# Kernel optimization log

Measured on AMD Instinct MI355X. Metric: run time of the kernel, lower is better.

Reference implementation:

```python
import jax, jax.numpy as jnp
import numpy as np

EPS_PRE = 1e-05   # constant added to raw scores in the torch module
EPS_NORM = 1e-12  # F.normalize default eps


def setup_inputs() -> dict:
    key = jax.random.key(0)
    kq, kk, kv = jax.random.split(key, 3)
    B, H, S, D = 2, 8, 2048, 64
    query = jax.random.normal(kq, (B, H, S, D), dtype=jnp.float32)
    keys = jax.random.normal(kk, (B, H, S, D), dtype=jnp.float32)
    vals = jax.random.normal(kv, (B, H, S, D), dtype=jnp.float32)
    # causal mask, broadcastable over batch and heads; mask==0 -> score zeroed
    mask = jnp.tril(jnp.ones((S, S), dtype=jnp.int32))[None, None, :, :]
    return {"query": query, "keys": keys, "vals": vals, "mask": mask}


def reference(query, keys, vals, mask):
    # preattn: [B,H,S,S]
    preattn = jnp.einsum("bhsd,bhtd->bhst", query, keys) + EPS_PRE
    preattn = jnp.where(mask == 0, 0.0, preattn)
    # F.normalize(dim=-1): x / max(||x||_2, eps)
    norm = jnp.sqrt(jnp.sum(preattn * preattn, axis=-1, keepdims=True))
    attn = preattn / jnp.maximum(norm, EPS_NORM)
    # dropout is identity in eval mode (reference baseline)
    out = jnp.einsum("bhst,bhtd->bhsd", attn, vals)
    return (out, attn)
```

## Files before the change

kernel.cpp:

```cpp
#include <hip/hip_runtime.h>

#define S_DIM 2048
#define D_DIM 64
#define EPS_PRE 1e-5f
#define EPS_NORM 1e-12f

typedef __attribute__((ext_vector_type(8))) short bf8;
typedef __attribute__((ext_vector_type(4))) float f32x4;

static __device__ __forceinline__ unsigned fbits(float x){ union{float f;unsigned u;}v; v.f=x; return v.u; }
static __device__ __forceinline__ float bcast(unsigned u){ union{unsigned u;float f;}v; v.u=u; return v.f; }

static __device__ __forceinline__ void split2(float x, unsigned short& h, unsigned short& l){
  unsigned u = fbits(x);
  h = (unsigned short)(u >> 16);
  float lo = x - bcast(u & 0xffff0000u);
  l = (unsigned short)(fbits(lo) >> 16);
}

static __device__ __forceinline__ void pack4f(float x0, float x1, float x2, float x3,
                                              uint2& hh, uint2& ll){
  unsigned u0=fbits(x0),u1=fbits(x1),u2=fbits(x2),u3=fbits(x3);
  hh.x = (u0>>16) | (u1 & 0xffff0000u);
  hh.y = (u2>>16) | (u3 & 0xffff0000u);
  float l0 = x0 - bcast(u0&0xffff0000u);
  float l1 = x1 - bcast(u1&0xffff0000u);
  float l2 = x2 - bcast(u2&0xffff0000u);
  float l3 = x3 - bcast(u3&0xffff0000u);
  ll.x = (fbits(l0)>>16) | (fbits(l1)&0xffff0000u);
  ll.y = (fbits(l2)>>16) | (fbits(l3)&0xffff0000u);
}

static __device__ __forceinline__ f32x4 mfma16(bf8 a, bf8 b, f32x4 c){
  return __builtin_amdgcn_mfma_f32_16x16x32_bf16(a, b, c, 0, 0, 0);
}

__global__ __launch_bounds__(256, 2)
void lka_fused(const float* __restrict__ Qg, const float* __restrict__ Kg,
               const float* __restrict__ Vg, float* __restrict__ Og,
               float* __restrict__ Ag)
{
  __shared__ short kThi[4096], kTlo[4096];
  __shared__ short vThi[4096], vTlo[4096];
  __shared__ short pHi [4096], pLo [4096];

  const int tid = threadIdx.x;
  const int wv  = tid >> 6;
  const int ln  = tid & 63;
  const int gq  = ln >> 4;
  const int i16 = ln & 15;

  const int blk = blockIdx.x;
  const int bh  = (blk & 7) | (((blk >> 3) & 1) << 3);
  const int qq  = blk >> 4;
  const int rbk = (qq < 16) ? qq : 47 - qq;
  const int s0  = rbk * 64;

  const float* Qb = Qg + (size_t)bh * (S_DIM * D_DIM);
  const float* Kb = Kg + (size_t)bh * (S_DIM * D_DIM);
  const float* Vb = Vg + (size_t)bh * (S_DIM * D_DIM);
  float* Ob = Og + (size_t)bh * (S_DIM * D_DIM);
  float* Ab = Ag + (size_t)bh * ((size_t)S_DIM * S_DIM);

  const int srow = s0 + wv * 16 + i16;

  bf8 qhi[2], qlo[2];
  #pragma unroll
  for (int ks = 0; ks < 2; ++ks) {
    const float* qp = Qb + (size_t)srow * D_DIM + ks * 32 + gq * 8;
    float4 a = *(const float4*)qp;
    float4 b = *(const float4*)(qp + 4);
    union { bf8 v; unsigned short h[8]; } H, L;
    float f0[8] = {a.x,a.y,a.z,a.w,b.x,b.y,b.z,b.w};
    #pragma unroll
    for (int j = 0; j < 8; ++j) split2(f0[j], H.h[j], L.h[j]);
    qhi[ks] = H.v; qlo[ks] = L.v;
  }

  {
    const int c0 = (rbk + 1) * 64;
    const int n4 = (S_DIM - c0) >> 2;
    const int r  = tid >> 2;
    float* rowp = Ab + (size_t)(s0 + r) * S_DIM + c0;
    float4 z = make_float4(0.f, 0.f, 0.f, 0.f);
    for (int c = (tid & 3); c < n4; c += 4)
      *(float4*)(rowp + 4*c) = z;
  }

  auto stageK = [&](int t0){
    const int t  = tid >> 2;
    const int db = (tid & 3) * 16;
    const float* kp = Kb + (size_t)(t0 + t) * D_DIM + db;
    #pragma unroll
    for (int c = 0; c < 4; ++c) {
      float4 kv = *(const float4*)(kp + 4*c);
      uint2 hh, ll; pack4f(kv.x, kv.y, kv.z, kv.w, hh, ll);
      const int idx = t*64 + ((db + 4*c) ^ ((t & 7) << 3));
      *(uint2*)&kThi[idx] = hh;
      *(uint2*)&kTlo[idx] = ll;
    }
  };
  auto stageV = [&](int t0){
    const int d  = (tid & 31) * 2;
    const int tb = (tid >> 5) * 8;
    float2 rr[8];
    #pragma unroll
    for (int k = 0; k < 8; ++k)
      rr[k] = *(const float2*)(Vb + (size_t)(t0 + tb + k) * D_DIM + d);
    #pragma unroll
    for (int dd = 0; dd < 2; ++dd) {
      union { bf8 v; unsigned short h[8]; } H, L;
      #pragma unroll
      for (int k = 0; k < 8; ++k) split2(dd ? rr[k].y : rr[k].x, H.h[k], L.h[k]);
      const int dc = d + dd;
      const int idx = dc*64 + (tb ^ ((dc & 7) << 3));
      *(bf8*)&vThi[idx] = H.v;
      *(bf8*)&vTlo[idx] = L.v;
    }
  };

  auto qkstep = [&](f32x4* acc){
    #pragma unroll
    for (int rf = 0; rf < 4; ++rf) acc[rf] = (f32x4){0.f,0.f,0.f,0.f};
    #pragma unroll
    for (int ks = 0; ks < 2; ++ks) {
      #pragma unroll
      for (int rf = 0; rf < 4; ++rf) {
        const int t   = rf*16 + i16;
        const int idx = t*64 + ((ks*32 + gq*8) ^ ((t & 7) << 3));
        bf8 ahi = *(const bf8*)&kThi[idx];
        bf8 alo = *(const bf8*)&kTlo[idx];
        acc[rf] = mfma16(ahi, qhi[ks], acc[rf]);
        acc[rf] = mfma16(alo, qhi[ks], acc[rf]);
        acc[rf] = mfma16(ahi, qlo[ks], acc[rf]);
      }
    }
  };

  float ssq = 0.f;
  for (int j = 0; j <= rbk; ++j) {
    __syncthreads();
    stageK(j * 64);
    __syncthreads();
    f32x4 acc[4];
    qkstep(acc);
    if (j == rbk) {
      #pragma unroll
      for (int rf = 0; rf < 4; ++rf)
        #pragma unroll
        for (int rg = 0; rg < 4; ++rg) {
          const int t = j*64 + rf*16 + gq*4 + rg;
          const float x = (t <= srow) ? (acc[rf][rg] + EPS_PRE) : 0.f;
          ssq += x * x;
        }
    } else {
      #pragma unroll
      for (int rf = 0; rf < 4; ++rf)
        #pragma unroll
        for (int rg = 0; rg < 4; ++rg) {
          const float x = acc[rf][rg] + EPS_PRE;
          ssq += x * x;
        }
    }
  }
  ssq += __shfl_xor(ssq, 16);
  ssq += __shfl_xor(ssq, 32);
  const float rinv = 1.f / fmaxf(sqrtf(ssq), EPS_NORM);

  f32x4 oacc[4];
  #pragma unroll
  for (int rf = 0; rf < 4; ++rf) oacc[rf] = (f32x4){0.f,0.f,0.f,0.f};

  const int pR = wv*16 + i16;

  for (int j = 0; j <= rbk; ++j) {
    __syncthreads();
    stageK(j * 64);
    stageV(j * 64);
    __syncthreads();

    f32x4 acc[4];
    qkstep(acc);

    #pragma unroll
    for (int rf = 0; rf < 4; ++rf) {
      f32x4 x;
      #pragma unroll
      for (int rg = 0; rg < 4; ++rg) {
        const int t = j*64 + rf*16 + gq*4 + rg;
        float v = acc[rf][rg] + EPS_PRE;
        if (j == rbk && t > srow) v = 0.f;
        x[rg] = v * rinv;
      }
      *(f32x4*)(Ab + (size_t)srow * S_DIM + j*64 + rf*16 + gq*4) = x;
      uint2 hh, ll; pack4f(x[0], x[1], x[2], x[3], hh, ll);
      const int pidx = pR*64 + ((rf*16 + gq*4) ^ ((pR & 7) << 3));
      *(uint2*)&pHi[pidx] = hh;
      *(uint2*)&pLo[pidx] = ll;
    }

    #pragma unroll
    for (int ks = 0; ks < 2; ++ks) {
      const int pi = pR*64 + ((ks*32 + gq*8) ^ ((pR & 7) << 3));
      bf8 bhi = *(const bf8*)&pHi[pi];
      bf8 blo = *(const bf8*)&pLo[pi];
      #pragma unroll
      for (int rfd = 0; rfd < 4; ++rfd) {
        const int dct = rfd*16 + i16;
        const int vi  = dct*64 + ((ks*32 + gq*8) ^ ((dct & 7) << 3));
        bf8 ahi = *(const bf8*)&vThi[vi];
        bf8 alo = *(const bf8*)&vTlo[vi];
        oacc[rfd] = mfma16(ahi, bhi, oacc[rfd]);
        oacc[rfd] = mfma16(alo, bhi, oacc[rfd]);
        oacc[rfd] = mfma16(ahi, blo, oacc[rfd]);
      }
    }
  }

  #pragma unroll
  for (int rfd = 0; rfd < 4; ++rfd)
    *(f32x4*)(Ob + (size_t)srow * D_DIM + rfd*16 + gq*4) = oacc[rfd];
}

extern "C" void kernel_launch(void* const* d_in, const int* in_sizes, int n_in,
                              void* d_out, int out_size, void* d_ws, size_t ws_size,
                              hipStream_t stream) {
  (void)in_sizes; (void)n_in; (void)out_size; (void)d_ws; (void)ws_size;
  const float* Q = (const float*)d_in[0];
  const float* K = (const float*)d_in[1];
  const float* V = (const float*)d_in[2];
  float* out  = (float*)d_out;
  float* attn = out + (size_t)2 * 8 * 2048 * 64;
  lka_fused<<<dim3(512), dim3(256), 0, stream>>>(Q, K, V, out, attn);
}
```

Measured before the change: 417.5 us.

## Split fused attention into norm and emit kernels with key-chunk work splitting

Splits the single fused kernel into two launches. The first computes per-row sum-of-squares over key chunks of up to 8 tiles and accumulates into a workspace with atomics; it also zeroes the upper triangle of the attention matrix. The second recomputes the scores, writes the normalized attention, and atomically accumulates partial outputs into a pre-zeroed output buffer. The goal is to balance the causal triangle across many more blocks (1280 instead of 512) and raise occupancy, in exchange for extra launches, memsets, and atomic traffic on the output and norm buffers.

```diff
diff --git a/kernel.cpp b/kernel.cpp
--- a/kernel.cpp
+++ b/kernel.cpp
@@ -2,8 +2,10 @@
 
 #define S_DIM 2048
 #define D_DIM 64
-#define EPS_PRE 1e-5f
+#define BH    16
+#define EPS_PRE  1e-5f
 #define EPS_NORM 1e-12f
+#define CT 8
 
 typedef __attribute__((ext_vector_type(8))) short bf8;
 typedef __attribute__((ext_vector_type(4))) float f32x4;
@@ -35,14 +37,21 @@
   return __builtin_amdgcn_mfma_f32_16x16x32_bf16(a, b, c, 0, 0, 0);
 }
 
-__global__ __launch_bounds__(256, 2)
-void lka_fused(const float* __restrict__ Qg, const float* __restrict__ Kg,
-               const float* __restrict__ Vg, float* __restrict__ Og,
-               float* __restrict__ Ag)
+static __device__ __forceinline__ void decode(int c, int& rb, int& ck, int& nk){
+  int g = 0;
+  while (c >= 4*(g+1)*(g+2)) ++g;
+  const int off = c - 4*g*(g+1);
+  nk = g + 1;
+  const int q = off / nk;
+  rb = g*8 + q;
+  ck = off - q*nk;
+}
+
+__global__ __launch_bounds__(256, 4)
+void lka_norm(const float* __restrict__ Qg, const float* __restrict__ Kg,
+              float* __restrict__ ssqg, float* __restrict__ Ag)
 {
   __shared__ short kThi[4096], kTlo[4096];
-  __shared__ short vThi[4096], vTlo[4096];
-  __shared__ short pHi [4096], pLo [4096];
 
   const int tid = threadIdx.x;
   const int wv  = tid >> 6;
@@ -51,18 +60,27 @@
   const int i16 = ln & 15;
 
   const int blk = blockIdx.x;
-  const int bh  = (blk & 7) | (((blk >> 3) & 1) << 3);
-  const int qq  = blk >> 4;
-  const int rbk = (qq < 16) ? qq : 47 - qq;
-  const int s0  = rbk * 64;
+  const int bh  = blk & 15;
+  int rb, ck, nk; decode(blk >> 4, rb, ck, nk);
+  const int s0 = rb * 64;
 
   const float* Qb = Qg + (size_t)bh * (S_DIM * D_DIM);
   const float* Kb = Kg + (size_t)bh * (S_DIM * D_DIM);
-  const float* Vb = Vg + (size_t)bh * (S_DIM * D_DIM);
-  float* Ob = Og + (size_t)bh * (S_DIM * D_DIM);
   float* Ab = Ag + (size_t)bh * ((size_t)S_DIM * S_DIM);
 
   const int srow = s0 + wv * 16 + i16;
+
+  {
+    const int zt0 = (rb + 1) + ((31 - rb) * ck) / nk;
+    const int zt1 = (rb + 1) + ((31 - rb) * (ck + 1)) / nk;
+    if (zt1 > zt0) {
+      const int r = tid >> 2;
+      float4* rowp = (float4*)(Ab + (size_t)(s0 + r) * S_DIM + zt0 * 64);
+      const int n4 = (zt1 - zt0) * 16;
+      float4 z = make_float4(0.f, 0.f, 0.f, 0.f);
+      for (int c4 = tid & 3; c4 < n4; c4 += 4) rowp[c4] = z;
+    }
+  }
 
   bf8 qhi[2], qlo[2];
   #pragma unroll
@@ -77,16 +95,6 @@
     qhi[ks] = H.v; qlo[ks] = L.v;
   }
 
-  {
-    const int c0 = (rbk + 1) * 64;
-    const int n4 = (S_DIM - c0) >> 2;
-    const int r  = tid >> 2;
-    float* rowp = Ab + (size_t)(s0 + r) * S_DIM + c0;
-    float4 z = make_float4(0.f, 0.f, 0.f, 0.f);
-    for (int c = (tid & 3); c < n4; c += 4)
-      *(float4*)(rowp + 4*c) = z;
-  }
-
   auto stageK = [&](int t0){
     const int t  = tid >> 2;
     const int db = (tid & 3) * 16;
@@ -98,24 +106,6 @@
       const int idx = t*64 + ((db + 4*c) ^ ((t & 7) << 3));
       *(uint2*)&kThi[idx] = hh;
       *(uint2*)&kTlo[idx] = ll;
-    }
-  };
-  auto stageV = [&](int t0){
-    const int d  = (tid & 31) * 2;
-    const int tb = (tid >> 5) * 8;
-    float2 rr[8];
-    #pragma unroll
-    for (int k = 0; k < 8; ++k)
-      rr[k] = *(const float2*)(Vb + (size_t)(t0 + tb + k) * D_DIM + d);
-    #pragma unroll
-    for (int dd = 0; dd < 2; ++dd) {
-      union { bf8 v; unsigned short h[8]; } H, L;
-      #pragma unroll
-      for (int k = 0; k < 8; ++k) split2(dd ? rr[k].y : rr[k].x, H.h[k], L.h[k]);
-      const int dc = d + dd;
-      const int idx = dc*64 + (tb ^ ((dc & 7) << 3));
-      *(bf8*)&vThi[idx] = H.v;
-      *(bf8*)&vTlo[idx] = L.v;
     }
   };
 
@@ -138,13 +128,15 @@
   };
 
   float ssq = 0.f;
-  for (int j = 0; j <= rbk; ++j) {
+  const int j0 = ck * CT;
+  const int j1 = min(j0 + CT, rb + 1);
+  for (int j = j0; j < j1; ++j) {
     __syncthreads();
     stageK(j * 64);
     __syncthreads();
     f32x4 acc[4];
     qkstep(acc);
-    if (j == rbk) {
+    if (j == rb) {
       #pragma unroll
       for (int rf = 0; rf < 4; ++rf)
         #pragma unroll
@@ -165,7 +157,103 @@
   }
   ssq += __shfl_xor(ssq, 16);
   ssq += __shfl_xor(ssq, 32);
-  const float rinv = 1.f / fmaxf(sqrtf(ssq), EPS_NORM);
+  if (gq == 0)
+    atomicAdd(&ssqg[bh * S_DIM + srow], ssq);
+}
+
+__global__ __launch_bounds__(256, 3)
+void lka_emit(const float* __restrict__ Qg, const float* __restrict__ Kg,
+              const float* __restrict__ Vg, const float* __restrict__ ssqg,
+              float* __restrict__ Og, float* __restrict__ Ag)
+{
+  __shared__ short kThi[4096], kTlo[4096];
+  __shared__ short vThi[4096], vTlo[4096];
+  __shared__ short pHi [4096], pLo [4096];
+
+  const int tid = threadIdx.x;
+  const int wv  = tid >> 6;
+  const int ln  = tid & 63;
+  const int gq  = ln >> 4;
+  const int i16 = ln & 15;
+
+  const int blk = blockIdx.x;
+  const int bh  = blk & 15;
+  int rb, ck, nk; decode(blk >> 4, rb, ck, nk);
+  (void)nk;
+  const int s0 = rb * 64;
+
+  const float* Qb = Qg + (size_t)bh * (S_DIM * D_DIM);
+  const float* Kb = Kg + (size_t)bh * (S_DIM * D_DIM);
+  const float* Vb = Vg + (size_t)bh * (S_DIM * D_DIM);
+  float* Ob = Og + (size_t)bh * (S_DIM * D_DIM);
+  float* Ab = Ag + (size_t)bh * ((size_t)S_DIM * S_DIM);
+
+  const int srow = s0 + wv * 16 + i16;
+
+  const float rinv = 1.f / fmaxf(sqrtf(ssqg[bh * S_DIM + srow]), EPS_NORM);
+
+  bf8 qhi[2], qlo[2];
+  #pragma unroll
+  for (int ks = 0; ks < 2; ++ks) {
+    const float* qp = Qb + (size_t)srow * D_DIM + ks * 32 + gq * 8;
+    float4 a = *(const float4*)qp;
+    float4 b = *(const float4*)(qp + 4);
+    union { bf8 v; unsigned short h[8]; } H, L;
+    float f0[8] = {a.x,a.y,a.z,a.w,b.x,b.y,b.z,b.w};
+    #pragma unroll
+    for (int j = 0; j < 8; ++j) split2(f0[j], H.h[j], L.h[j]);
+    qhi[ks] = H.v; qlo[ks] = L.v;
+  }
+
+  auto stageK = [&](int t0){
+    const int t  = tid >> 2;
+    const int db = (tid & 3) * 16;
+    const float* kp = Kb + (size_t)(t0 + t) * D_DIM + db;
+    #pragma unroll
+    for (int c = 0; c < 4; ++c) {
+      float4 kv = *(const float4*)(kp + 4*c);
+      uint2 hh, ll; pack4f(kv.x, kv.y, kv.z, kv.w, hh, ll);
+      const int idx = t*64 + ((db + 4*c) ^ ((t & 7) << 3));
+      *(uint2*)&kThi[idx] = hh;
+      *(uint2*)&kTlo[idx] = ll;
+    }
+  };
+  auto stageV = [&](int t0){
+    const int d  = (tid & 31) * 2;
+    const int tb = (tid >> 5) * 8;
+    float2 rr[8];
+    #pragma unroll
+    for (int k = 0; k < 8; ++k)
+      rr[k] = *(const float2*)(Vb + (size_t)(t0 + tb + k) * D_DIM + d);
+    #pragma unroll
+    for (int dd = 0; dd < 2; ++dd) {
+      union { bf8 v; unsigned short h[8]; } H, L;
+      #pragma unroll
+      for (int k = 0; k < 8; ++k) split2(dd ? rr[k].y : rr[k].x, H.h[k], L.h[k]);
+      const int dc = d + dd;
+      const int idx = dc*64 + (tb ^ ((dc & 7) << 3));
+      *(bf8*)&vThi[idx] = H.v;
+      *(bf8*)&vTlo[idx] = L.v;
+    }
+  };
+
+  auto qkstep = [&](f32x4* acc){
+    #pragma unroll
+    for (int rf = 0; rf < 4; ++rf) acc[rf] = (f32x4){0.f,0.f,0.f,0.f};
+    #pragma unroll
+    for (int ks = 0; ks < 2; ++ks) {
+      #pragma unroll
+      for (int rf = 0; rf < 4; ++rf) {
+        const int t   = rf*16 + i16;
+        const int idx = t*64 + ((ks*32 + gq*8) ^ ((t & 7) << 3));
+        bf8 ahi = *(const bf8*)&kThi[idx];
+        bf8 alo = *(const bf8*)&kTlo[idx];
+        acc[rf] = mfma16(ahi, qhi[ks], acc[rf]);
+        acc[rf] = mfma16(alo, qhi[ks], acc[rf]);
+        acc[rf] = mfma16(ahi, qlo[ks], acc[rf]);
+      }
+    }
+  };
 
   f32x4 oacc[4];
   #pragma unroll
@@ -173,7 +261,9 @@
 
   const int pR = wv*16 + i16;
 
-  for (int j = 0; j <= rbk; ++j) {
+  const int j0 = ck * CT;
+  const int j1 = min(j0 + CT, rb + 1);
+  for (int j = j0; j < j1; ++j) {
     __syncthreads();
     stageK(j * 64);
     stageV(j * 64);
@@ -189,7 +279,7 @@
       for (int rg = 0; rg < 4; ++rg) {
         const int t = j*64 + rf*16 + gq*4 + rg;
         float v = acc[rf][rg] + EPS_PRE;
-        if (j == rbk && t > srow) v = 0.f;
+        if (j == rb && t > srow) v = 0.f;
         x[rg] = v * rinv;
       }
       *(f32x4*)(Ab + (size_t)srow * S_DIM + j*64 + rf*16 + gq*4) = x;
@@ -219,17 +309,26 @@
 
   #pragma unroll
   for (int rfd = 0; rfd < 4; ++rfd)
-    *(f32x4*)(Ob + (size_t)srow * D_DIM + rfd*16 + gq*4) = oacc[rfd];
+    #pragma unroll
+    for (int rg = 0; rg < 4; ++rg)
+      atomicAdd(&Ob[(size_t)srow * D_DIM + rfd*16 + gq*4 + rg], oacc[rfd][rg]);
 }
 
 extern "C" void kernel_launch(void* const* d_in, const int* in_sizes, int n_in,
                               void* d_out, int out_size, void* d_ws, size_t ws_size,
                               hipStream_t stream) {
-  (void)in_sizes; (void)n_in; (void)out_size; (void)d_ws; (void)ws_size;
+  (void)in_sizes; (void)n_in; (void)out_size; (void)ws_size;
   const float* Q = (const float*)d_in[0];
   const float* K = (const float*)d_in[1];
   const float* V = (const float*)d_in[2];
   float* out  = (float*)d_out;
-  float* attn = out + (size_t)2 * 8 * 2048 * 64;
-  lka_fused<<<dim3(512), dim3(256), 0, stream>>>(Q, K, V, out, attn);
-}
+  float* attn = out + (size_t)BH * S_DIM * D_DIM;
+  float* ssq  = (float*)d_ws;
+
+  hipMemsetAsync(ssq, 0, (size_t)BH * S_DIM * sizeof(float), stream);
+  hipMemsetAsync(out, 0, (size_t)BH * S_DIM * D_DIM * sizeof(float), stream);
+
+  const int nblk = BH * 80;
+  lka_norm<<<dim3(nblk), dim3(256), 0, stream>>>(Q, K, ssq, attn);
+  lka_emit<<<dim3(nblk), dim3(256), 0, stream>>>(Q, K, V, ssq, out, attn);
+}
```

Result: faster. 388.4 us (-7.0%).
